# Kernel optimization log

Hardware: AMD Instinct MI355X
Metric: run time of the kernel (lower is better)

The kernel has to match this reference:

```python
import jax, jax.numpy as jnp
import numpy as np

B = 16
NS = [2048, 1024, 512, 256]
K = 12
GROUPS = 64
OUT = 1024
EPS = 1e-5


def setup_inputs() -> dict:
    key = jax.random.key(0)
    ks = iter(jax.random.split(key, 40))
    d = {}
    for i, n in enumerate(NS):
        d[f"fs{i}"] = jax.random.normal(next(ks), (B, n, 256), jnp.float32)
        d[f"xs{i}"] = jax.random.normal(next(ks), (B, n, 3), jnp.float32)
        ct = 1024 if i == 0 else 256
        d[f"ft{i}"] = jax.random.normal(next(ks), (B, n, ct), jnp.float32)
        d[f"xt{i}"] = jax.random.normal(next(ks), (B, n, 3), jnp.float32)
    d["Ws"] = jax.random.normal(next(ks), (4, OUT, 256), jnp.float32) * 0.05
    d["bWs"] = jax.random.normal(next(ks), (4, OUT), jnp.float32) * 0.05
    d["gs"] = jax.random.uniform(next(ks), (4, OUT), jnp.float32, 0.5, 1.5)
    d["bes"] = jax.random.normal(next(ks), (4, OUT), jnp.float32) * 0.05
    d["mus"] = jax.random.normal(next(ks), (4, OUT), jnp.float32) * 0.05
    d["vs"] = jax.random.uniform(next(ks), (4, OUT), jnp.float32, 0.5, 1.5)
    d["Wt0"] = jax.random.normal(next(ks), (OUT, 1024), jnp.float32) * 0.02
    d["Wt123"] = jax.random.normal(next(ks), (3, OUT, 256), jnp.float32) * 0.05
    d["bWt"] = jax.random.normal(next(ks), (4, OUT), jnp.float32) * 0.05
    d["gt"] = jax.random.uniform(next(ks), (4, OUT), jnp.float32, 0.5, 1.5)
    d["bet"] = jax.random.normal(next(ks), (4, OUT), jnp.float32) * 0.05
    d["mut"] = jax.random.normal(next(ks), (4, OUT), jnp.float32) * 0.05
    d["vt"] = jax.random.uniform(next(ks), (4, OUT), jnp.float32, 0.5, 1.5)
    return d


def fps(xyz, m):
    # furthest point sampling starting from index 0 (as in pointnet2_utils)
    b, n, _ = xyz.shape
    idxs = jnp.zeros((b, m), jnp.int32)
    d2 = jnp.full((b, n), 1e10, xyz.dtype)
    last = jnp.zeros((b,), jnp.int32)

    def body(i, st):
        idxs, d2, last = st
        lx = jnp.take_along_axis(xyz, last[:, None, None], axis=1)  # [b,1,3]
        d = jnp.sum((xyz - lx) ** 2, axis=-1)  # [b,n]
        d2 = jnp.minimum(d2, d)
        nxt = jnp.argmax(d2, axis=-1).astype(jnp.int32)
        return idxs.at[:, i].set(nxt), d2, nxt

    idxs, _, _ = jax.lax.fori_loop(1, m, body, (idxs, d2, last))
    return idxs


def gather_points(feat, idx):
    # feat [b,n,c], idx [b,...] -> [b,...,c]
    flat = idx.reshape(idx.shape[0], -1)
    out = jnp.take_along_axis(feat, flat[..., None], axis=1)
    return out.reshape(idx.shape + (feat.shape[-1],))


def knn_point(k, xyz, query):
    # squared pairwise distances [b,m,n]; k smallest (== torch.topk largest=False)
    d = (jnp.sum(query ** 2, -1, keepdims=True)
         - 2.0 * jnp.einsum('bmd,bnd->bmn', query, xyz)
         + jnp.sum(xyz ** 2, -1)[:, None, :])
    _, idx = jax.lax.top_k(-d, k)
    return idx.astype(jnp.int32)


def graph_op(grouped, w, b, g, be, mu, v):
    # grouped [B,M,K,C]; kernel-1 Conv1d == channel matmul; eval-mode BN; ReLU; max over K
    x = jnp.einsum('bmkc,oc->bmko', grouped, w) + b
    x = (x - mu) * (g * jax.lax.rsqrt(v + EPS)) + be
    x = jax.nn.relu(x)
    return jnp.max(x, axis=2)  # [B,M,O]


def reference(fs0, xs0, ft0, xt0, fs1, xs1, ft1, xt1, fs2, xs2, ft2, xt2,
              fs3, xs3, ft3, xt3, Ws, bWs, gs, bes, mus, vs,
              Wt0, Wt123, bWt, gt, bet, mut, vt):
    fs_list = [fs0, fs1, fs2, fs3]
    xs_list = [xs0, xs1, xs2, xs3]
    ft_list = [ft0, ft1, ft2, ft3]
    xt_list = [xt0, xt1, xt2, xt3]

    fps_idx = fps(xt_list[-1], GROUPS)              # [B,G]
    new_xyz = gather_points(xt_list[-1], fps_idx)   # [B,G,3]

    out_s, out_t = [], []
    for i in range(4):
        idx_t = knn_point(K, xt_list[i], new_xyz)   # [B,G,K]
        grp_t = gather_points(ft_list[i], idx_t)    # [B,G,K,Ct]
        idx_s = knn_point(K, xs_list[i], new_xyz)
        grp_s = gather_points(fs_list[i], idx_s)    # [B,G,K,256]
        wt = Wt0 if i == 0 else Wt123[i - 1]
        out_s.append(graph_op(grp_s, Ws[i], bWs[i], gs[i], bes[i], mus[i], vs[i]))
        out_t.append(graph_op(grp_t, wt, bWt[i], gt[i], bet[i], mut[i], vt[i]))
    return (tuple(out_s), tuple(out_t))
```

## Files before the change

### kernel.cpp

```cpp
#include <hip/hip_runtime.h>
#include <hip/hip_bf16.h>

#define DEVI __device__ __forceinline__

typedef __attribute__((ext_vector_type(8))) short bf16x8;
typedef __attribute__((ext_vector_type(16))) float f32x16;
typedef __attribute__((ext_vector_type(4))) unsigned int u32x4;
typedef __attribute__((ext_vector_type(4))) float fl4;

DEVI unsigned short f2bf(float f) {
  union { float f; unsigned u; } x; x.f = f;
  unsigned r = (x.u + 0x7fffu + ((x.u >> 16) & 1u)) >> 16;
  return (unsigned short)r;
}

DEVI unsigned cvtpk(float lo, float hi) {
  unsigned r;
  asm("v_cvt_pk_bf16_f32 %0, %1, %2" : "=v"(r) : "v"(lo), "v"(hi));
  return r;
}

DEVI float fadd3(float a, float b, float c) {
  return __fadd_rn(__fadd_rn(a, b), c);
}


__global__ __launch_bounds__(256) void prep_fps_kernel(
    const float* __restrict__ Ws, const float* __restrict__ Wt0,
    const float* __restrict__ Wt123,
    const float* __restrict__ bWs, const float* __restrict__ gs,
    const float* __restrict__ bes, const float* __restrict__ mus,
    const float* __restrict__ vs,
    const float* __restrict__ bWt, const float* __restrict__ gt,
    const float* __restrict__ bet, const float* __restrict__ mut,
    const float* __restrict__ vt, const float* __restrict__ xt3,
    char* __restrict__ wbf, float* __restrict__ bnA, float* __restrict__ bnB,
    float* __restrict__ newxyz) {
  if (blockIdx.x >= 11296u) {
    const int b = blockIdx.x - 11296;
    const int t = threadIdx.x;
    if (t >= 64) return;
    const float* P = xt3 + (size_t)b * 256 * 3;
    float px[4], py[4], pz[4], d2[4];
#pragma unroll
    for (int j = 0; j < 4; ++j) {
      int p = t + 64 * j;
      px[j] = P[p * 3 + 0]; py[j] = P[p * 3 + 1]; pz[j] = P[p * 3 + 2];
      d2[j] = 1e10f;
    }
    float* NX = newxyz + (size_t)b * 64 * 3;
    float cx = __shfl(px[0], 0), cy = __shfl(py[0], 0), cz = __shfl(pz[0], 0);
    if (t == 0) { NX[0] = cx; NX[1] = cy; NX[2] = cz; }
    for (int i = 1; i < 64; ++i) {
      float bv = -1.0f; int bi = 0;
#pragma unroll
      for (int j = 0; j < 4; ++j) {
        float dx = __fsub_rn(px[j], cx), dy = __fsub_rn(py[j], cy),
              dz = __fsub_rn(pz[j], cz);
        float d = fadd3(__fmul_rn(dx, dx), __fmul_rn(dy, dy), __fmul_rn(dz, dz));
        d2[j] = fminf(d2[j], d);
        int p = t + 64 * j;
        if (j == 0) { bv = d2[0]; bi = t; }
        else if (d2[j] > bv) { bv = d2[j]; bi = p; }
      }
#pragma unroll
      for (int off = 32; off >= 1; off >>= 1) {
        float ov = __shfl_xor(bv, off);
        int oi = __shfl_xor(bi, off);
        if (ov > bv || (ov == bv && oi < bi)) { bv = ov; bi = oi; }
      }
      int s = bi;
      int owner = s & 63, slot = s >> 6;
      float sx = slot == 0 ? px[0] : slot == 1 ? px[1] : slot == 2 ? px[2] : px[3];
      float sy = slot == 0 ? py[0] : slot == 1 ? py[1] : slot == 2 ? py[2] : py[3];
      float sz = slot == 0 ? pz[0] : slot == 1 ? pz[1] : slot == 2 ? pz[2] : pz[3];
      cx = __shfl(sx, owner); cy = __shfl(sy, owner); cz = __shfl(sz, owner);
      if (t == 0) { NX[i * 3 + 0] = cx; NX[i * 3 + 1] = cy; NX[i * 3 + 2] = cz; }
    }
    return;
  }
  const unsigned id = blockIdx.x * 256u + threadIdx.x;
  const unsigned WN = 2883584u;
  if (id < WN) {
    float val; unsigned c, o, k, woffE;
    if (id < 1048576u) {
      c = id >> 18; unsigned rem = id & 262143u;
      o = rem >> 8; k = rem & 255u; val = Ws[id]; woffE = c << 18;
    } else if (id < 2097152u) {
      c = 4u; unsigned rem = id - 1048576u;
      o = rem >> 10; k = rem & 1023u; val = Wt0[rem]; woffE = 1048576u;
    } else {
      unsigned rem = id - 2097152u; unsigned cc = rem >> 18;
      c = 5u + cc; unsigned r2 = rem & 262143u;
      o = r2 >> 8; k = r2 & 255u; val = Wt123[rem];
      woffE = 2097152u + (cc << 18);
    }
    unsigned NKT = (c == 4u) ? 16u : 4u;
    unsigned ntile = o >> 8, op = o & 255u, kt = k >> 6, kl = k & 63u;
    unsigned byteoff = (woffE << 1) + ((ntile * NKT + kt) << 15) +
                       (kl >> 3) * 4096u + op * 16u + (kl & 7u) * 2u;
    *(unsigned short*)(wbf + byteoff) = f2bf(val);
  } else {
    unsigned r = id - WN;
    unsigned c = r >> 10, o = r & 1023u;
    float g, bW, mu, v, be;
    if (c < 4u) { g = gs[r]; bW = bWs[r]; mu = mus[r]; v = vs[r]; be = bes[r]; }
    else {
      unsigned r2 = (c - 4u) * 1024u + o;
      g = gt[r2]; bW = bWt[r2]; mu = mut[r2]; v = vt[r2]; be = bet[r2];
    }
    float A = g / sqrtf(v + 1e-5f);
    float B = (bW - mu) * A + be;
    bnA[r] = A; bnB[r] = B;
  }
}

template <int NJ>
DEVI void knn_run(int lane, const float* __restrict__ X, float qx, float qy,
                  float qz, float qq, int* __restrict__ out) {
  float d2[NJ];
#pragma unroll
  for (int j = 0; j < NJ; ++j) {
    int pi = lane + 64 * j;
    float x = X[pi * 3 + 0], y = X[pi * 3 + 1], z = X[pi * 3 + 2];
    float xx = fadd3(__fmul_rn(x, x), __fmul_rn(y, y), __fmul_rn(z, z));
    float dot = fadd3(__fmul_rn(qx, x), __fmul_rn(qy, y), __fmul_rn(qz, z));
    d2[j] = __fadd_rn(__fsub_rn(qq, __fmul_rn(2.0f, dot)), xx);
  }
  for (int kk = 0; kk < 12; ++kk) {
    float bv = d2[0]; int bi = lane;
#pragma unroll
    for (int j = 1; j < NJ; ++j) {
      if (d2[j] < bv) { bv = d2[j]; bi = lane + 64 * j; }
    }
#pragma unroll
    for (int off = 1; off <= 32; off <<= 1) {
      float ov = __shfl_xor(bv, off);
      int oi = __shfl_xor(bi, off);
      if (ov < bv || (ov == bv && oi < bi)) { bv = ov; bi = oi; }
    }
    if (lane == 0) out[kk] = bi;
#pragma unroll
    for (int j = 0; j < NJ; ++j)
      if (bi == lane + 64 * j) d2[j] = 3.4e38f;
  }
}

struct KnnP { const float* xyz[8]; };

__global__ __launch_bounds__(256) void knn_kernel(KnnP p,
                                                  const float* __restrict__ newxyz,
                                                  int* __restrict__ idxbuf) {
  const int q = blockIdx.x * 4 + (threadIdx.x >> 6);
  const int lane = threadIdx.x & 63;
  const int c = q >> 10, b = (q >> 6) & 15, g = q & 63;
  const int n = 2048 >> (c & 3);
  const float* X = p.xyz[c] + (size_t)b * n * 3;
  const float* qp = newxyz + ((size_t)b * 64 + g) * 3;
  float qx = qp[0], qy = qp[1], qz = qp[2];
  float qq = fadd3(__fmul_rn(qx, qx), __fmul_rn(qy, qy), __fmul_rn(qz, qz));
  int* out = idxbuf + (size_t)q * 12;
  switch (c & 3) {
    case 0: knn_run<32>(lane, X, qx, qy, qz, qq, out); break;
    case 1: knn_run<16>(lane, X, qx, qy, qz, qq, out); break;
    case 2: knn_run<8>(lane, X, qx, qy, qz, qq, out); break;
    default: knn_run<4>(lane, X, qx, qy, qz, qq, out); break;
  }
}

struct GImgP {
  const float* feat[8];
  int n[8];
  int K[8];
  int NKT[8];
  unsigned goffB[8];
  unsigned base[9];
};

__global__ __launch_bounds__(256) void gather_img_kernel(
    GImgP p, const int* __restrict__ idxbuf, char* __restrict__ grouped) {
  const unsigned blk = blockIdx.x;
  int c = 0;
#pragma unroll
  for (int j = 1; j < 8; ++j) if (blk >= p.base[j]) c = j;
  const unsigned local = blk - p.base[c];
  const int NKT = p.NKT[c];
  const int mtile = local / NKT;
  const int kt = local - mtile * NKT;
  const int row = threadIdx.x;
  const int gl = row >> 4, kslot = row & 15;
  const int ke = (kslot < 12) ? kslot : 0;
  const int group = mtile * 16 + gl;
  const int b = group >> 6;
  const int pidx = idxbuf[(size_t)c * 12288 + group * 12 + ke];
  const int K = p.K[c];
  const float* src = p.feat[c] + ((size_t)b * p.n[c] + pidx) * K + kt * 64;
  char* dst = grouped + p.goffB[c] + ((size_t)(mtile * NKT + kt)) * 32768u +
              row * 16;
#pragma unroll
  for (int s = 0; s < 8; ++s) {
    fl4 v0 = *reinterpret_cast<const fl4*>(src + s * 8);
    fl4 v1 = *reinterpret_cast<const fl4*>(src + s * 8 + 4);
    u32x4 w;
    w[0] = cvtpk(v0[0], v0[1]);
    w[1] = cvtpk(v0[2], v0[3]);
    w[2] = cvtpk(v1[0], v1[1]);
    w[3] = cvtpk(v1[2], v1[3]);
    *reinterpret_cast<u32x4*>(dst + s * 4096) = w;
  }
}

struct GemmPR {
  unsigned goff[8]; unsigned woff[8]; unsigned outoff[8];
  unsigned bnoff[8]; int K[8];
};

#define GLOAD_LDS16(gsrc, ldsdst)                                              \
  __builtin_amdgcn_global_load_lds(                                            \
      (const __attribute__((address_space(1))) void*)(gsrc),                   \
      (__attribute__((address_space(3))) void*)(ldsdst), 16, 0, 0)

__global__ __launch_bounds__(512, 2) void gemm_pers_kernel(
    const char* __restrict__ grouped, const char* __restrict__ wbf,
    const float* __restrict__ bnA, const float* __restrict__ bnB,
    float* __restrict__ out, GemmPR p) {
  extern __shared__ char smem[];
  const int bid = blockIdx.x;
  const int xcd = bid & 7, slot = bid >> 3;
  const int rem = (xcd << 5) | slot;
  const int mtile = rem >> 2, ntile = rem & 3;
  const int tid = threadIdx.x;
  const int lane = tid & 63, wid = tid >> 6;
  const int wr = wid >> 2, wc = wid & 3;

  const int aoff = (lane >> 5) * 4096 + (wr * 128 + (lane & 31)) * 16;
  const int boff = (lane >> 5) * 4096 + (wc * 64 + (lane & 31)) * 16;

  f32x16 acc[4][2];
#pragma unroll
  for (int j = 0; j < 4; ++j)
#pragma unroll
    for (int nn = 0; nn < 2; ++nn)
#pragma unroll
      for (int e = 0; e < 16; ++e) acc[j][nn][e] = 0.f;

  auto stageA = [&](int par, const char* src) {
    char* dst = smem + par * 65536;
#pragma unroll
    for (int it = 0; it < 4; ++it)
      GLOAD_LDS16(src + (it * 512 + tid) * 16, dst + (it * 512 + wid * 64) * 16);
  };
  auto stageB = [&](int par, const char* src) {
    char* dst = smem + par * 65536 + 32768;
#pragma unroll
    for (int it = 0; it < 4; ++it)
      GLOAD_LDS16(src + (it * 512 + tid) * 16, dst + (it * 512 + wid * 64) * 16);
  };

  int nkt = p.K[0] >> 6;
  const char* Ac = grouped + p.goff[0] + (size_t)mtile * nkt * 32768;
  const char* Bc = wbf + p.woff[0] + (size_t)ntile * nkt * 32768;

  stageA(0, Ac); stageB(0, Bc);
  stageA(1, Ac + 32768); stageB(1, Bc + 32768);
  asm volatile("s_waitcnt vmcnt(8)" ::: "memory");
  __builtin_amdgcn_s_barrier();

  int gs = 0;
  int par = 0;
  for (int zi = 0; zi < 8; ++zi) {
    nkt = p.K[zi] >> 6;
    const char* An = nullptr;
    const char* Bn = nullptr;
    if (zi < 7) {
      int nktN = p.K[zi + 1] >> 6;
      An = grouped + p.goff[zi + 1] + (size_t)mtile * nktN * 32768;
      Bn = wbf + p.woff[zi + 1] + (size_t)ntile * nktN * 32768;
    }
    for (int kt = 0; kt < nkt; ++kt, ++gs, par ^= 1) {
      const char* As = smem + par * 65536;
      const char* Bs = As + 32768;
      const bool do_stage = (gs + 2 < 44);
      const char* sA = nullptr;
      const char* sB = nullptr;
      if (do_stage) {
        int k2 = kt + 2;
        if (k2 < nkt) { sA = Ac + (size_t)k2 * 32768; sB = Bc + (size_t)k2 * 32768; }
        else { int r2 = k2 - nkt; sA = An + (size_t)r2 * 32768; sB = Bn + (size_t)r2 * 32768; }
      }
      bf16x8 af[2][4], bv[4][2];

#pragma unroll
      for (int ks2 = 0; ks2 < 2; ++ks2)
#pragma unroll
        for (int j = 0; j < 4; ++j)
          af[ks2][j] = *reinterpret_cast<const bf16x8*>(
              As + ks2 * 8192 + j * 512 + aoff);
#pragma unroll
      for (int ks = 0; ks < 4; ++ks)
#pragma unroll
        for (int nn = 0; nn < 2; ++nn)
          bv[ks][nn] = *reinterpret_cast<const bf16x8*>(
              Bs + ks * 8192 + nn * 512 + boff);
      __builtin_amdgcn_s_barrier();
      asm volatile("s_waitcnt lgkmcnt(0)" ::: "memory");
      __builtin_amdgcn_sched_barrier(0);
      __builtin_amdgcn_s_setprio(1);
#pragma unroll
      for (int ks2 = 0; ks2 < 2; ++ks2)
#pragma unroll
        for (int j = 0; j < 4; ++j)
#pragma unroll
          for (int nn = 0; nn < 2; ++nn)
            acc[j][nn] = __builtin_amdgcn_mfma_f32_32x32x16_bf16(
                af[ks2][j], bv[ks2][nn], acc[j][nn], 0, 0, 0);
      __builtin_amdgcn_s_setprio(0);
      if (do_stage) stageB(par, sB);
      __builtin_amdgcn_s_barrier();

#pragma unroll
      for (int ks2 = 0; ks2 < 2; ++ks2)
#pragma unroll
        for (int j = 0; j < 4; ++j)
          af[ks2][j] = *reinterpret_cast<const bf16x8*>(
              As + 16384 + ks2 * 8192 + j * 512 + aoff);
      __builtin_amdgcn_s_barrier();
      asm volatile("s_waitcnt lgkmcnt(0)" ::: "memory");
      __builtin_amdgcn_sched_barrier(0);
      __builtin_amdgcn_s_setprio(1);
#pragma unroll
      for (int ks2 = 0; ks2 < 2; ++ks2)
#pragma unroll
        for (int j = 0; j < 4; ++j)
#pragma unroll
          for (int nn = 0; nn < 2; ++nn)
            acc[j][nn] = __builtin_amdgcn_mfma_f32_32x32x16_bf16(
                af[ks2][j], bv[2 + ks2][nn], acc[j][nn], 0, 0, 0);
      __builtin_amdgcn_s_setprio(0);
      if (do_stage) stageA(par, sA);
      if (gs + 1 < 44) {
        if (do_stage)
          asm volatile("s_waitcnt vmcnt(8)" ::: "memory");
        else
          asm volatile("s_waitcnt vmcnt(0)" ::: "memory");
      }
      __builtin_amdgcn_sched_barrier(0);
      __builtin_amdgcn_s_barrier();
    }

    const float* bA = bnA + p.bnoff[zi];
    const float* bB = bnB + p.bnoff[zi];
    float* O = out + (size_t)p.outoff[zi];
#pragma unroll
    for (int nn = 0; nn < 2; ++nn) {
      int colb = ntile * 256 + wc * 64 + nn * 32 + (lane & 31);
      float sA = bA[colb], sB = bB[colb];
#pragma unroll
      for (int j = 0; j < 4; ++j) {
#pragma unroll
        for (int h = 0; h < 2; ++h) {
          float v = acc[j][nn][8 * h];
#pragma unroll
          for (int e = 1; e < 8; ++e) v = fmaxf(v, acc[j][nn][8 * h + e]);
          v = fmaxf(v, __shfl_xor(v, 32));
          if (lane < 32) {
            int grp = mtile * 16 + wr * 8 + j * 2 + h;
            float val = fmaf(v, sA, sB);
            O[(size_t)grp * 1024 + colb] = fmaxf(val, 0.f);
          }
        }
      }
    }
#pragma unroll
    for (int j = 0; j < 4; ++j)
#pragma unroll
      for (int nn = 0; nn < 2; ++nn)
#pragma unroll
        for (int e = 0; e < 16; ++e) acc[j][nn][e] = 0.f;
    Ac = An;
    Bc = Bn;
  }
}

extern "C" void kernel_launch(void* const* d_in, const int* in_sizes, int n_in,
                              void* d_out, int out_size, void* d_ws,
                              size_t ws_size, hipStream_t stream) {
  (void)in_sizes; (void)n_in; (void)out_size; (void)ws_size;
  const float *fs[4], *xs[4], *ft[4], *xt[4];
  for (int i = 0; i < 4; ++i) {
    fs[i] = (const float*)d_in[4 * i + 0];
    xs[i] = (const float*)d_in[4 * i + 1];
    ft[i] = (const float*)d_in[4 * i + 2];
    xt[i] = (const float*)d_in[4 * i + 3];
  }
  const float* Ws = (const float*)d_in[16];
  const float* bWs = (const float*)d_in[17];
  const float* gs = (const float*)d_in[18];
  const float* bes = (const float*)d_in[19];
  const float* mus = (const float*)d_in[20];
  const float* vs = (const float*)d_in[21];
  const float* Wt0 = (const float*)d_in[22];
  const float* Wt123 = (const float*)d_in[23];
  const float* bWt = (const float*)d_in[24];
  const float* gt = (const float*)d_in[25];
  const float* bet = (const float*)d_in[26];
  const float* mut = (const float*)d_in[27];
  const float* vt = (const float*)d_in[28];

  char* ws = (char*)d_ws;
  float* newxyz = (float*)(ws + 0);
  int* idxbuf = (int*)(ws + 16384);
  float* bnA = (float*)(ws + 409600);
  float* bnB = (float*)(ws + 442368);
  char* wbf = ws + 475136;
  char* grouped = ws + 6242304;

  static const int NSarr[4] = {2048, 1024, 512, 256};
  const unsigned goffB[8] = {0u,        8388608u,  16777216u, 25165824u,
                             33554432u, 67108864u, 75497472u, 83886080u};
  const unsigned woffB[8] = {0u,       524288u,  1048576u, 1572864u,
                             2097152u, 4194304u, 4718592u, 5242880u};

  prep_fps_kernel<<<11312, 256, 0, stream>>>(Ws, Wt0, Wt123, bWs, gs, bes, mus,
                                             vs, bWt, gt, bet, mut, vt, xt[3],
                                             wbf, bnA, bnB, newxyz);

  KnnP kp;
  for (int i = 0; i < 4; ++i) {
    kp.xyz[i] = xs[i];
    kp.xyz[4 + i] = xt[i];
  }
  knn_kernel<<<2048, 256, 0, stream>>>(kp, newxyz, idxbuf);

  GImgP gp;
  unsigned cum = 0;
  for (int c = 0; c < 8; ++c) {
    int scale = c & 3;
    gp.feat[c] = (c < 4) ? fs[scale] : ft[scale];
    gp.n[c] = NSarr[scale];
    gp.K[c] = (c == 4) ? 1024 : 256;
    gp.NKT[c] = (c == 4) ? 16 : 4;
    gp.goffB[c] = goffB[c];
    gp.base[c] = cum;
    cum += 64u * (unsigned)gp.NKT[c];
  }
  gp.base[8] = cum;
  gather_img_kernel<<<cum, 256, 0, stream>>>(gp, idxbuf, grouped);

  static const int co[8] = {0, 1, 2, 3, 5, 6, 7, 4};
  GemmPR mp;
  for (int zi = 0; zi < 8; ++zi) {
    int c = co[zi];
    mp.goff[zi] = goffB[c]; mp.woff[zi] = woffB[c];
    mp.outoff[zi] = (unsigned)c * 1048576u;
    mp.bnoff[zi] = (unsigned)c * 1024u;
    mp.K[zi] = (c == 4) ? 1024 : 256;
  }
  (void)hipFuncSetAttribute((const void*)gemm_pers_kernel,
                            hipFuncAttributeMaxDynamicSharedMemorySize, 131072);
  gemm_pers_kernel<<<256, 512, 131072, stream>>>(grouped, wbf, bnA, bnB,
                                                 (float*)d_out, mp);
}
```

Baseline: 223.5 us.

## Replace depth-2 split-stage GEMM pipeline with simple one-ahead double buffering

The hand-tuned two-stage-ahead prefetch is replaced by a simpler scheme. It used split A/B staging into the just-consumed half-buffers, explicit vmcnt waits, extra barriers and setprio. Now the next k-tile is staged into the other buffer at the top of each iteration, and one __syncthreads sits at the end. This cuts barrier count and scheduling constraints but shortens prefetch distance. The compiler-inserted waits for __syncthreads may also fully drain the global loads each iteration, reducing overlap.

```diff
diff --git a/kernel.cpp b/kernel.cpp
--- a/kernel.cpp
+++ b/kernel.cpp
@@ -261,13 +261,11 @@
   const char* Ac = grouped + p.goff[0] + (size_t)mtile * nkt * 32768;
   const char* Bc = wbf + p.woff[0] + (size_t)ntile * nkt * 32768;
 
-  stageA(0, Ac); stageB(0, Bc);
-  stageA(1, Ac + 32768); stageB(1, Bc + 32768);
-  asm volatile("s_waitcnt vmcnt(8)" ::: "memory");
-  __builtin_amdgcn_s_barrier();
+  stageA(0, Ac);
+  stageB(0, Bc);
+  __syncthreads();
 
   int gs = 0;
-  int par = 0;
   for (int zi = 0; zi < 8; ++zi) {
     nkt = p.K[zi] >> 6;
     const char* An = nullptr;
@@ -277,19 +275,27 @@
       An = grouped + p.goff[zi + 1] + (size_t)mtile * nktN * 32768;
       Bn = wbf + p.woff[zi + 1] + (size_t)ntile * nktN * 32768;
     }
-    for (int kt = 0; kt < nkt; ++kt, ++gs, par ^= 1) {
+    for (int kt = 0; kt < nkt; ++kt, ++gs) {
+      const int par = gs & 1;
       const char* As = smem + par * 65536;
       const char* Bs = As + 32768;
-      const bool do_stage = (gs + 2 < 44);
-      const char* sA = nullptr;
-      const char* sB = nullptr;
-      if (do_stage) {
-        int k2 = kt + 2;
-        if (k2 < nkt) { sA = Ac + (size_t)k2 * 32768; sB = Bc + (size_t)k2 * 32768; }
-        else { int r2 = k2 - nkt; sA = An + (size_t)r2 * 32768; sB = Bn + (size_t)r2 * 32768; }
+
+      if (gs + 1 < 44) {
+        int k1 = kt + 1;
+        const char* sA, * sB;
+        if (k1 < nkt) { sA = Ac + (size_t)k1 * 32768; sB = Bc + (size_t)k1 * 32768; }
+        else { sA = An; sB = Bn; }
+        stageA(par ^ 1, sA);
+        stageB(par ^ 1, sB);
       }
-      bf16x8 af[2][4], bv[4][2];
-
+
+      bf16x8 bv[4][2], af[2][4];
+#pragma unroll
+      for (int ks = 0; ks < 4; ++ks)
+#pragma unroll
+        for (int nn = 0; nn < 2; ++nn)
+          bv[ks][nn] = *reinterpret_cast<const bf16x8*>(
+              Bs + ks * 8192 + nn * 512 + boff);
 #pragma unroll
       for (int ks2 = 0; ks2 < 2; ++ks2)
 #pragma unroll
@@ -297,16 +303,6 @@
           af[ks2][j] = *reinterpret_cast<const bf16x8*>(
               As + ks2 * 8192 + j * 512 + aoff);
 #pragma unroll
-      for (int ks = 0; ks < 4; ++ks)
-#pragma unroll
-        for (int nn = 0; nn < 2; ++nn)
-          bv[ks][nn] = *reinterpret_cast<const bf16x8*>(
-              Bs + ks * 8192 + nn * 512 + boff);
-      __builtin_amdgcn_s_barrier();
-      asm volatile("s_waitcnt lgkmcnt(0)" ::: "memory");
-      __builtin_amdgcn_sched_barrier(0);
-      __builtin_amdgcn_s_setprio(1);
-#pragma unroll
       for (int ks2 = 0; ks2 < 2; ++ks2)
 #pragma unroll
         for (int j = 0; j < 4; ++j)
@@ -314,20 +310,12 @@
           for (int nn = 0; nn < 2; ++nn)
             acc[j][nn] = __builtin_amdgcn_mfma_f32_32x32x16_bf16(
                 af[ks2][j], bv[ks2][nn], acc[j][nn], 0, 0, 0);
-      __builtin_amdgcn_s_setprio(0);
-      if (do_stage) stageB(par, sB);
-      __builtin_amdgcn_s_barrier();
-
 #pragma unroll
       for (int ks2 = 0; ks2 < 2; ++ks2)
 #pragma unroll
         for (int j = 0; j < 4; ++j)
           af[ks2][j] = *reinterpret_cast<const bf16x8*>(
               As + 16384 + ks2 * 8192 + j * 512 + aoff);
-      __builtin_amdgcn_s_barrier();
-      asm volatile("s_waitcnt lgkmcnt(0)" ::: "memory");
-      __builtin_amdgcn_sched_barrier(0);
-      __builtin_amdgcn_s_setprio(1);
 #pragma unroll
       for (int ks2 = 0; ks2 < 2; ++ks2)
 #pragma unroll
@@ -336,16 +324,8 @@
           for (int nn = 0; nn < 2; ++nn)
             acc[j][nn] = __builtin_amdgcn_mfma_f32_32x32x16_bf16(
                 af[ks2][j], bv[2 + ks2][nn], acc[j][nn], 0, 0, 0);
-      __builtin_amdgcn_s_setprio(0);
-      if (do_stage) stageA(par, sA);
-      if (gs + 1 < 44) {
-        if (do_stage)
-          asm volatile("s_waitcnt vmcnt(8)" ::: "memory");
-        else
-          asm volatile("s_waitcnt vmcnt(0)" ::: "memory");
-      }
-      __builtin_amdgcn_sched_barrier(0);
-      __builtin_amdgcn_s_barrier();
+
+      __syncthreads();
     }
 
     const float* bA = bnA + p.bnoff[zi];
```

Measured after the change: 218.4 us. 2.3% less time.
